# Performance work log

Measured on AMD Instinct MI355X. Metric: run time of the kernel, lower is better.

Reference implementation:

```python
import jax, jax.numpy as jnp
import numpy as np

NUM_EMBEDDINGS = 1024
EMBEDDING_DIM = 64
COMMIT_COST = 0.25


def setup_inputs() -> dict:
    key = jax.random.key(0)
    k1, k2 = jax.random.split(key)
    latent = jax.random.normal(k1, (32, EMBEDDING_DIM, 32, 32), dtype=jnp.float32)
    embedding_weight = jax.random.normal(k2, (NUM_EMBEDDINGS, EMBEDDING_DIM), dtype=jnp.float32)
    return {"latent": latent, "embedding_weight": embedding_weight}


def reference(latent, embedding_weight):
    # rearrange 'b n j d -> b j d n'; n == embedding_dim
    lat = jnp.transpose(latent, (0, 2, 3, 1))  # [b, j, d, n]
    flat = lat.reshape(-1, EMBEDDING_DIM)      # [T, D]
    # squared-euclidean distances [T, K]
    distances = (
        jnp.sum(flat ** 2, axis=1, keepdims=True)
        + jnp.sum(embedding_weight ** 2, axis=1)
        - 2.0 * flat @ embedding_weight.T
    )
    idx = jnp.argmin(distances, axis=1)                         # [T]
    encodings = jax.nn.one_hot(idx, NUM_EMBEDDINGS, dtype=flat.dtype)  # [T, K]
    quantized_flat = embedding_weight[idx]                      # gather == encodings @ W
    quantized = quantized_flat.reshape(lat.shape)               # [b, j, d, n]

    e_latent_loss = jnp.mean((jax.lax.stop_gradient(quantized) - lat) ** 2)
    loss = COMMIT_COST * e_latent_loss

    # straight-through estimator
    quantized_st = lat + jax.lax.stop_gradient(quantized - lat)

    avg_probs = jnp.mean(encodings, axis=0)
    perplexity = jnp.exp(-jnp.sum(avg_probs * jnp.log(avg_probs + 1e-10)))

    # rearrange back 'b j d n -> b n j d'
    quantized_out = jnp.transpose(quantized_st, (0, 3, 1, 2))
    return quantized_out, loss, perplexity, encodings, distances
```

## Files before the change

### kernel.cpp

```cpp
#include <hip/hip_runtime.h>
#include <cfloat>

#define T_TOTAL 32768
#define DIM 64
#define KCODES 1024

static constexpr long long OFF_Q    = 0;
static constexpr long long OFF_LOSS = 2097152;
static constexpr long long OFF_PERP = 2097153;
static constexpr long long OFF_ENC  = 2097154;
static constexpr long long OFF_DIST = 2097154LL + 33554432LL;


__global__ __launch_bounds__(256) void vq_prep_kernel(const float* __restrict__ W,
                                                      float* __restrict__ ww,
                                                      float* __restrict__ WT) {
    const int tid = threadIdx.x;
    if (blockIdx.x < 256) {
        const int lane = tid & 63;
        const int code = blockIdx.x * 4 + (tid >> 6);
        float v = W[code * DIM + lane];
        float s = v * v;
        #pragma unroll
        for (int off = 32; off > 0; off >>= 1)
            s += __shfl_down(s, off, 64);
        if (lane == 0) ww[code] = s;
    } else {
        const int n = blockIdx.x - 256;
        #pragma unroll
        for (int i = 0; i < 4; ++i) {
            int k = i * 256 + tid;
            WT[n * KCODES + k] = W[k * DIM + n];
        }
    }
}

__global__ __launch_bounds__(256, 3) void vq_main_kernel(const float* __restrict__ lat,
                                                         const float* __restrict__ W,
                                                         const float* __restrict__ ww,
                                                         const float* __restrict__ WT,
                                                         float* __restrict__ out,
                                                         int* __restrict__ counts,
                                                         float* __restrict__ lossSum) {
    __shared__ float xT[64 * 64];
    __shared__ float wS[32 * 256];
    __shared__ float xx[64];
    __shared__ int   selIdx[64];

    const int tid = threadIdx.x;
    const int tx  = tid & 31;
    const int ty  = tid >> 5;
    const int t0  = blockIdx.x * 64;
    const long long base = (long long)(t0 >> 10) * 65536 + (long long)(t0 & 1023);

    #pragma unroll
    for (int i = 0; i < 16; ++i) {
        int e  = i * 256 + tid;
        int n  = e >> 6;
        int tl = e & 63;
        xT[n * 64 + tl] = lat[base + (long long)n * 1024 + tl];
    }
    __syncthreads();
    if (tid < 64) {
        float s = 0.f;
        #pragma unroll 8
        for (int n = 0; n < 64; ++n) {
            float v = xT[n * 64 + tid];
            s = fmaf(v, v, s);
        }
        xx[tid] = s;
    }

    float minV[8];
    int   minI[8];
    #pragma unroll
    for (int r = 0; r < 8; ++r) { minV[r] = FLT_MAX; minI[r] = 0; }

    float* __restrict__ distOut = out + OFF_DIST;

    for (int c = 0; c < 4; ++c) {
        float acc[8][8];
        #pragma unroll
        for (int r = 0; r < 8; ++r)
            #pragma unroll
            for (int k = 0; k < 8; ++k) acc[r][k] = 0.f;

        for (int h = 0; h < 2; ++h) {
            __syncthreads();
            #pragma unroll
            for (int i = 0; i < 8; ++i) {
                int e2 = i * 256 + tid;
                int n  = e2 >> 6;
                int k4 = e2 & 63;
                *(float4*)&wS[n * 256 + k4 * 4] =
                    *(const float4*)&WT[(h * 32 + n) * KCODES + c * 256 + k4 * 4];
            }
            __syncthreads();

            #pragma unroll 4
            for (int nn = 0; nn < 32; ++nn) {
                const float* xrow = &xT[(h * 32 + nn) * 64];
                const float* wrow = &wS[nn * 256];
                float4 a0 = *(const float4*)&xrow[ty * 4];
                float4 a1 = *(const float4*)&xrow[32 + ty * 4];
                float4 b0 = *(const float4*)&wrow[tx * 4];
                float4 b1 = *(const float4*)&wrow[128 + tx * 4];
                float ar[8] = {a0.x, a0.y, a0.z, a0.w, a1.x, a1.y, a1.z, a1.w};
                float br[8] = {b0.x, b0.y, b0.z, b0.w, b1.x, b1.y, b1.z, b1.w};
                #pragma unroll
                for (int r = 0; r < 8; ++r)
                    #pragma unroll
                    for (int k = 0; k < 8; ++k)
                        acc[r][k] = fmaf(ar[r], br[k], acc[r][k]);
            }
        }

        const int kb0 = c * 256 + tx * 4;
        float wr[8];
        #pragma unroll
        for (int k = 0; k < 8; ++k)
            wr[k] = ww[kb0 + (k >> 2) * 128 + (k & 3)];
        #pragma unroll
        for (int r = 0; r < 8; ++r) {
            const int row = (r >> 2) * 32 + ty * 4 + (r & 3);
            const float xxr = xx[row];
            float d[8];
            #pragma unroll
            for (int k = 0; k < 8; ++k) {
                d[k] = (xxr + wr[k]) - 2.f * acc[r][k];
                int ki = kb0 + (k >> 2) * 128 + (k & 3);
                if (d[k] < minV[r]) { minV[r] = d[k]; minI[r] = ki; }
            }
            const long long ro = (long long)(t0 + row) * KCODES + kb0;
            *(float2*)&distOut[ro]           = make_float2(d[0], d[1]);
            *(float2*)&distOut[ro + 2]       = make_float2(d[2], d[3]);
            *(float2*)&distOut[ro + 128]     = make_float2(d[4], d[5]);
            *(float2*)&distOut[ro + 130]     = make_float2(d[6], d[7]);
        }
    }

    __syncthreads();
    float* redV = wS;
    int*   redI = (int*)(wS + 64 * 33);
    #pragma unroll
    for (int r = 0; r < 8; ++r) {
        const int row = (r >> 2) * 32 + ty * 4 + (r & 3);
        redV[row * 33 + tx] = minV[r];
        redI[row * 33 + tx] = minI[r];
    }
    __syncthreads();
    if (tid < 64) {
        float best = redV[tid * 33];
        int   bi   = redI[tid * 33];
        #pragma unroll
        for (int s = 1; s < 32; ++s) {
            float v  = redV[tid * 33 + s];
            int   i2 = redI[tid * 33 + s];
            if (v < best || (v == best && i2 < bi)) { best = v; bi = i2; }
        }
        selIdx[tid] = bi;
        atomicAdd(&counts[bi], 1);
    }
    __syncthreads();

    float* qS = wS;
    #pragma unroll
    for (int i = 0; i < 16; ++i) {
        int e   = i * 256 + tid;
        int row = e >> 6;
        int n   = e & 63;
        qS[row * 65 + n] = W[selIdx[row] * DIM + n];
    }
    __syncthreads();

    float ls = 0.f;
    #pragma unroll
    for (int i = 0; i < 4; ++i) {
        int e2  = i * 256 + tid;
        int n   = e2 >> 4;
        int tl0 = (e2 & 15) * 4;
        float q0 = qS[(tl0 + 0) * 65 + n];
        float q1 = qS[(tl0 + 1) * 65 + n];
        float q2 = qS[(tl0 + 2) * 65 + n];
        float q3 = qS[(tl0 + 3) * 65 + n];
        float x0 = xT[n * 64 + tl0 + 0];
        float x1 = xT[n * 64 + tl0 + 1];
        float x2 = xT[n * 64 + tl0 + 2];
        float x3 = xT[n * 64 + tl0 + 3];
        *(float4*)&out[OFF_Q + base + (long long)n * 1024 + tl0] = make_float4(q0, q1, q2, q3);
        float e0 = q0 - x0; ls = fmaf(e0, e0, ls);
        float e1 = q1 - x1; ls = fmaf(e1, e1, ls);
        float e2d = q2 - x2; ls = fmaf(e2d, e2d, ls);
        float e3 = q3 - x3; ls = fmaf(e3, e3, ls);
    }
    #pragma unroll
    for (int off = 32; off > 0; off >>= 1)
        ls += __shfl_down(ls, off, 64);
    if ((tid & 63) == 0) atomicAdd(lossSum, ls);

    float* __restrict__ enc = out + OFF_ENC;
    for (int i = 0; i < 128; ++i) {
        int e2  = i * 256 + tid;
        int row = e2 >> 9;
        int k2  = (e2 & 511) * 2;
        int sel = selIdx[row];
        float2 v;
        v.x = (k2     == sel) ? 1.f : 0.f;
        v.y = (k2 + 1 == sel) ? 1.f : 0.f;
        *(float2*)&enc[(long long)(t0 + row) * KCODES + k2] = v;
    }
}

__global__ __launch_bounds__(1024) void vq_finalize_kernel(const int* __restrict__ counts,
                                                           const float* __restrict__ lossSum,
                                                           float* __restrict__ out) {
    __shared__ float red[16];
    const int tid = threadIdx.x;
    float p = (float)counts[tid] * (1.0f / 32768.0f);
    float term = p * logf(p + 1e-10f);
    #pragma unroll
    for (int off = 32; off > 0; off >>= 1)
        term += __shfl_down(term, off, 64);
    if ((tid & 63) == 0) red[tid >> 6] = term;
    __syncthreads();
    if (tid == 0) {
        float s = 0.f;
        #pragma unroll
        for (int i = 0; i < 16; ++i) s += red[i];
        out[OFF_PERP] = expf(-s);
        out[OFF_LOSS] = 0.25f * lossSum[0] * (1.0f / 2097152.0f);
    }
}

extern "C" void kernel_launch(void* const* d_in, const int* in_sizes, int n_in,
                              void* d_out, int out_size, void* d_ws, size_t ws_size,
                              hipStream_t stream) {
    (void)in_sizes; (void)n_in; (void)out_size; (void)ws_size;
    const float* lat = (const float*)d_in[0];
    const float* W   = (const float*)d_in[1];
    float* out = (float*)d_out;

    int*   counts  = (int*)d_ws;
    float* ww      = (float*)((char*)d_ws + 4096);
    float* lossSum = (float*)((char*)d_ws + 8192);
    float* WT      = (float*)((char*)d_ws + 12288);

    hipMemsetAsync(d_ws, 0, 8192 + 16, stream);

    vq_prep_kernel<<<320, 256, 0, stream>>>(W, ww, WT);
    vq_main_kernel<<<512, 256, 0, stream>>>(lat, W, ww, WT, out, counts, lossSum);
    vq_finalize_kernel<<<1, 1024, 0, stream>>>(counts, lossSum, out);
}
```

Baseline: 341.0 us.

## Double-buffer codebook tiles via direct-to-LDS loads and interleave encoding zero-fill

Codebook tiles are now loaded with global_load_lds straight into LDS, double-buffered, so the next tile's fetch overlaps the current FMA work. Per-thread accumulators grow to 8x16 over two 512-code chunks, and ww is cached in shared memory. Zeroing of the one-hot encoding rows is spread across the compute loop, and the single 1.0 per row is written at the end, so output stores overlap compute instead of forming a separate tail. The larger register and LDS footprint lowers the occupancy hint from 3 to 2 blocks per CU.

New measurement: 338.2 us. Within noise of the previous version (-0.8%).

```diff
diff --git a/kernel.cpp b/kernel.cpp
--- a/kernel.cpp
+++ b/kernel.cpp
@@ -11,6 +11,14 @@
 static constexpr long long OFF_ENC  = 2097154;
 static constexpr long long OFF_DIST = 2097154LL + 33554432LL;
 
+
+#define AS1 __attribute__((address_space(1)))
+#define AS3 __attribute__((address_space(3)))
+
+__device__ __forceinline__ void gld16(const float* g, float* l) {
+    __builtin_amdgcn_global_load_lds((const AS1 unsigned int*)g,
+                                     (AS3 unsigned int*)l, 16, 0, 0);
+}
 
 __global__ __launch_bounds__(256) void vq_prep_kernel(const float* __restrict__ W,
                                                       float* __restrict__ ww,
@@ -35,7 +43,7 @@
     }
 }
 
-__global__ __launch_bounds__(256, 3) void vq_main_kernel(const float* __restrict__ lat,
+__global__ __launch_bounds__(256, 2) void vq_main_kernel(const float* __restrict__ lat,
                                                          const float* __restrict__ W,
                                                          const float* __restrict__ ww,
                                                          const float* __restrict__ WT,
@@ -43,7 +51,8 @@
                                                          int* __restrict__ counts,
                                                          float* __restrict__ lossSum) {
     __shared__ float xT[64 * 64];
-    __shared__ float wS[32 * 256];
+    __shared__ float wS[2][8 * 512];
+    __shared__ float wwS[KCODES];
     __shared__ float xx[64];
     __shared__ int   selIdx[64];
 
@@ -52,15 +61,23 @@
     const int ty  = tid >> 5;
     const int t0  = blockIdx.x * 64;
     const long long base = (long long)(t0 >> 10) * 65536 + (long long)(t0 & 1023);
-
-    #pragma unroll
-    for (int i = 0; i < 16; ++i) {
-        int e  = i * 256 + tid;
-        int n  = e >> 6;
-        int tl = e & 63;
-        xT[n * 64 + tl] = lat[base + (long long)n * 1024 + tl];
-    }
-    __syncthreads();
+    const int wbase = (tid & 192) * 4;
+
+    #pragma unroll
+    for (int i = 0; i < 4; ++i) {
+        const int e = i * 256 + tid;
+        gld16(&lat[base + (long long)(e >> 4) * 1024 + (e & 15) * 4],
+              &xT[i * 1024 + wbase]);
+    }
+    #pragma unroll
+    for (int i = 0; i < 4; ++i) {
+        const int e = i * 256 + tid;
+        gld16(&WT[(e >> 7) * KCODES + (e & 127) * 4],
+              &wS[0][i * 1024 + wbase]);
+    }
+    *(float4*)&wwS[tid * 4] = *(const float4*)&ww[tid * 4];
+    __syncthreads();
+
     if (tid < 64) {
         float s = 0.f;
         #pragma unroll 8
@@ -76,72 +93,107 @@
     #pragma unroll
     for (int r = 0; r < 8; ++r) { minV[r] = FLT_MAX; minI[r] = 0; }
 
+    float acc[8][16];
     float* __restrict__ distOut = out + OFF_DIST;
-
-    for (int c = 0; c < 4; ++c) {
-        float acc[8][8];
-        #pragma unroll
-        for (int r = 0; r < 8; ++r)
-            #pragma unroll
-            for (int k = 0; k < 8; ++k) acc[r][k] = 0.f;
-
-        for (int h = 0; h < 2; ++h) {
-            __syncthreads();
-            #pragma unroll
-            for (int i = 0; i < 8; ++i) {
-                int e2 = i * 256 + tid;
-                int n  = e2 >> 6;
-                int k4 = e2 & 63;
-                *(float4*)&wS[n * 256 + k4 * 4] =
-                    *(const float4*)&WT[(h * 32 + n) * KCODES + c * 256 + k4 * 4];
-            }
-            __syncthreads();
-
-            #pragma unroll 4
-            for (int nn = 0; nn < 32; ++nn) {
-                const float* xrow = &xT[(h * 32 + nn) * 64];
-                const float* wrow = &wS[nn * 256];
-                float4 a0 = *(const float4*)&xrow[ty * 4];
-                float4 a1 = *(const float4*)&xrow[32 + ty * 4];
-                float4 b0 = *(const float4*)&wrow[tx * 4];
-                float4 b1 = *(const float4*)&wrow[128 + tx * 4];
-                float ar[8] = {a0.x, a0.y, a0.z, a0.w, a1.x, a1.y, a1.z, a1.w};
-                float br[8] = {b0.x, b0.y, b0.z, b0.w, b1.x, b1.y, b1.z, b1.w};
-                #pragma unroll
-                for (int r = 0; r < 8; ++r)
-                    #pragma unroll
-                    for (int k = 0; k < 8; ++k)
-                        acc[r][k] = fmaf(ar[r], br[k], acc[r][k]);
-            }
-        }
-
-        const int kb0 = c * 256 + tx * 4;
-        float wr[8];
-        #pragma unroll
-        for (int k = 0; k < 8; ++k)
-            wr[k] = ww[kb0 + (k >> 2) * 128 + (k & 3)];
-        #pragma unroll
-        for (int r = 0; r < 8; ++r) {
-            const int row = (r >> 2) * 32 + ty * 4 + (r & 3);
-            const float xxr = xx[row];
-            float d[8];
-            #pragma unroll
-            for (int k = 0; k < 8; ++k) {
-                d[k] = (xxr + wr[k]) - 2.f * acc[r][k];
-                int ki = kb0 + (k >> 2) * 128 + (k & 3);
-                if (d[k] < minV[r]) { minV[r] = d[k]; minI[r] = ki; }
-            }
-            const long long ro = (long long)(t0 + row) * KCODES + kb0;
-            *(float2*)&distOut[ro]           = make_float2(d[0], d[1]);
-            *(float2*)&distOut[ro + 2]       = make_float2(d[2], d[3]);
-            *(float2*)&distOut[ro + 128]     = make_float2(d[4], d[5]);
-            *(float2*)&distOut[ro + 130]     = make_float2(d[6], d[7]);
-        }
-    }
-
-    __syncthreads();
-    float* redV = wS;
-    int*   redI = (int*)(wS + 64 * 33);
+    float* __restrict__ enc     = out + OFF_ENC;
+    const float4 z4 = make_float4(0.f, 0.f, 0.f, 0.f);
+
+    for (int p = 0; p < 16; ++p) {
+        const int c   = p >> 3;
+        const int q   = p & 7;
+        const int buf = p & 1;
+
+        if (p < 15) {
+            const int pn = p + 1;
+            const float* srcb = WT + (pn & 7) * (8 * KCODES) + (pn >> 3) * 512;
+            float* dstb = &wS[pn & 1][0];
+            #pragma unroll
+            for (int i = 0; i < 4; ++i) {
+                const int e = i * 256 + tid;
+                gld16(&srcb[(e >> 7) * KCODES + (e & 127) * 4],
+                      &dstb[i * 1024 + wbase]);
+            }
+        }
+
+        {
+            float* pz = enc + (long long)(t0 + p * 4) * KCODES;
+            if (tid < 255) {
+                float* pf = pz + 2 + tid * 4;
+                *(float4*)(pf)        = z4;
+                *(float4*)(pf + 1024) = z4;
+                *(float4*)(pf + 2048) = z4;
+                *(float4*)(pf + 3072) = z4;
+            } else {
+                #pragma unroll
+                for (int rr = 0; rr < 4; ++rr) {
+                    *(float2*)(pz + rr * 1024)        = make_float2(0.f, 0.f);
+                    *(float2*)(pz + rr * 1024 + 1022) = make_float2(0.f, 0.f);
+                }
+            }
+        }
+
+        if (q == 0) {
+            #pragma unroll
+            for (int r = 0; r < 8; ++r)
+                #pragma unroll
+                for (int k = 0; k < 16; ++k) acc[r][k] = 0.f;
+        }
+
+        #pragma unroll 2
+        for (int nn = 0; nn < 8; ++nn) {
+            const float* xrow = &xT[(q * 8 + nn) * 64];
+            const float* wrow = &wS[buf][nn * 512];
+            float4 a0 = *(const float4*)&xrow[ty * 4];
+            float4 a1 = *(const float4*)&xrow[32 + ty * 4];
+            float4 b0 = *(const float4*)&wrow[tx * 4];
+            float4 b1 = *(const float4*)&wrow[128 + tx * 4];
+            float4 b2 = *(const float4*)&wrow[256 + tx * 4];
+            float4 b3 = *(const float4*)&wrow[384 + tx * 4];
+            float ar[8]  = {a0.x, a0.y, a0.z, a0.w, a1.x, a1.y, a1.z, a1.w};
+            float br[16] = {b0.x, b0.y, b0.z, b0.w, b1.x, b1.y, b1.z, b1.w,
+                            b2.x, b2.y, b2.z, b2.w, b3.x, b3.y, b3.z, b3.w};
+            #pragma unroll
+            for (int r = 0; r < 8; ++r)
+                #pragma unroll
+                for (int k = 0; k < 16; ++k)
+                    acc[r][k] = fmaf(ar[r], br[k], acc[r][k]);
+        }
+
+        if (q == 7) {
+            const int kb = c * 512 + tx * 4;
+            float wr[16];
+            #pragma unroll
+            for (int qq = 0; qq < 4; ++qq) {
+                float4 w4 = *(const float4*)&wwS[kb + qq * 128];
+                wr[qq*4+0] = w4.x; wr[qq*4+1] = w4.y; wr[qq*4+2] = w4.z; wr[qq*4+3] = w4.w;
+            }
+            #pragma unroll
+            for (int r = 0; r < 8; ++r) {
+                const int row = (r >> 2) * 32 + ty * 4 + (r & 3);
+                const float xxr = xx[row];
+                const long long ro = (long long)(t0 + row) * KCODES + kb;
+                #pragma unroll
+                for (int qq = 0; qq < 4; ++qq) {
+                    float d0 = (xxr + wr[qq*4+0]) - 2.f * acc[r][qq*4+0];
+                    float d1 = (xxr + wr[qq*4+1]) - 2.f * acc[r][qq*4+1];
+                    float d2 = (xxr + wr[qq*4+2]) - 2.f * acc[r][qq*4+2];
+                    float d3 = (xxr + wr[qq*4+3]) - 2.f * acc[r][qq*4+3];
+                    const int k0 = kb + qq * 128;
+                    if (d0 < minV[r]) { minV[r] = d0; minI[r] = k0;     }
+                    if (d1 < minV[r]) { minV[r] = d1; minI[r] = k0 + 1; }
+                    if (d2 < minV[r]) { minV[r] = d2; minI[r] = k0 + 2; }
+                    if (d3 < minV[r]) { minV[r] = d3; minI[r] = k0 + 3; }
+                    *(float2*)&distOut[ro + qq * 128]     = make_float2(d0, d1);
+                    *(float2*)&distOut[ro + qq * 128 + 2] = make_float2(d2, d3);
+                }
+            }
+        }
+        __syncthreads();
+    }
+
+    float* wSf  = &wS[0][0];
+    float* redV = wSf;
+    int*   redI = (int*)(wSf + 64 * 33);
     #pragma unroll
     for (int r = 0; r < 8; ++r) {
         const int row = (r >> 2) * 32 + ty * 4 + (r & 3);
@@ -163,7 +215,7 @@
     }
     __syncthreads();
 
-    float* qS = wS;
+    float* qS = wSf;
     #pragma unroll
     for (int i = 0; i < 16; ++i) {
         int e   = i * 256 + tid;
@@ -198,17 +250,8 @@
         ls += __shfl_down(ls, off, 64);
     if ((tid & 63) == 0) atomicAdd(lossSum, ls);
 
-    float* __restrict__ enc = out + OFF_ENC;
-    for (int i = 0; i < 128; ++i) {
-        int e2  = i * 256 + tid;
-        int row = e2 >> 9;
-        int k2  = (e2 & 511) * 2;
-        int sel = selIdx[row];
-        float2 v;
-        v.x = (k2     == sel) ? 1.f : 0.f;
-        v.y = (k2 + 1 == sel) ? 1.f : 0.f;
-        *(float2*)&enc[(long long)(t0 + row) * KCODES + k2] = v;
-    }
+    if (tid < 64)
+        enc[(long long)(t0 + tid) * KCODES + selIdx[tid]] = 1.f;
 }
 
 __global__ __launch_bounds__(1024) void vq_finalize_kernel(const int* __restrict__ counts,
@@ -235,7 +278,8 @@
 extern "C" void kernel_launch(void* const* d_in, const int* in_sizes, int n_in,
                               void* d_out, int out_size, void* d_ws, size_t ws_size,
                               hipStream_t stream) {
-    (void)in_sizes; (void)n_in; (void)out_size; (void)ws_size;
+    (void)in_sizes; (void)n_in; (void)n_in;
+    (void)out_size; (void)ws_size;
     const float* lat = (const float*)d_in[0];
     const float* W   = (const float*)d_in[1];
     float* out = (float*)d_out;
```
